# Kernel tuning notes

Hardware: AMD Instinct MI355X
Metric: run time of the kernel (lower is better)

Reference implementation:

```python
import jax, jax.numpy as jnp
import numpy as np

WINDOW_SIZE = 11
C1 = (0.01 * 255) ** 2
C2 = (0.03 * 255) ** 2


def _make_window():
    # NOTE: faithful to the torch module: Gaussian with 2*sigma^2 = 4, UNNORMALIZED.
    x = np.arange(WINDOW_SIZE)
    g = np.exp(-((x - WINDOW_SIZE // 2) ** 2) / float(2 * 2)).astype(np.float32)
    w2d = np.outer(g, g)  # [11, 11]
    return jnp.asarray(w2d)[None, None, :, :]  # OIHW = [1, 1, 11, 11]


def _conv(x, w):
    pad = WINDOW_SIZE // 2
    return jax.lax.conv_general_dilated(
        x, w, window_strides=(1, 1), padding=[(pad, pad), (pad, pad)],
        dimension_numbers=('NCHW', 'OIHW', 'NCHW'))


def setup_inputs() -> dict:
    key = jax.random.key(0)
    k1, k2 = jax.random.split(key)
    shape = (32, 1, 512, 512)
    img1 = jax.random.uniform(k1, shape, dtype=jnp.float32)
    img2 = jax.random.uniform(k2, shape, dtype=jnp.float32)
    return {"img1": img1, "img2": img2}


def reference(img1, img2):
    w = _make_window()
    mu1 = _conv(img1, w)
    mu2 = _conv(img2, w)
    mu1_sq = mu1 * mu1
    mu2_sq = mu2 * mu2
    mu1_mu2 = mu1 * mu2
    sigma1_sq = _conv(img1 * img1, w) - mu1_sq
    sigma2_sq = _conv(img2 * img2, w) - mu2_sq
    sigma12 = _conv(img1 * img2, w) - mu1_mu2
    ssim_map = ((2 * mu1_mu2 + C1) * (2 * sigma12 + C2)) / (
        (mu1_sq + mu2_sq + C1) * (sigma1_sq + sigma2_sq + C2))
    return jnp.mean((1.0 - ssim_map) / 2.0)
```

## Files before the change

kernel.cpp:

```cpp
#include <hip/hip_runtime.h>
#include <hip/hip_fp16.h>


#define IMGW 512
#define IMGH 512
#define NIMG 32
#define TW 32
#define TH 64
#define IN_H 74
#define IN_W 44
#define NPIX (IN_H * IN_W)
#define NCHUNK (IN_H * 11)
#define NBX 16
#define NBY 8
#define NBLOCKS (NBX * NBY * NIMG)
#define LOWCH 512
#define LOWROWS 42

typedef __attribute__((address_space(1))) const uint32_t ga_u32;
typedef __attribute__((address_space(3))) uint32_t ls_u32;

__device__ __forceinline__ void load16_lds(const float* g, float* l) {
  __builtin_amdgcn_global_load_lds((ga_u32*)g, (ls_u32*)l, 16, 0, 0);
}
__device__ __forceinline__ __half2 h2_of(uint32_t w) {
  return __builtin_bit_cast(__half2, w);
}
__device__ __forceinline__ uint32_t u_of(__half2 h) {
  return __builtin_bit_cast(uint32_t, h);
}
__device__ __forceinline__ void lds_barrier() {
  asm volatile("s_waitcnt lgkmcnt(0)" ::: "memory");
  __builtin_amdgcn_s_barrier();
  __builtin_amdgcn_sched_barrier(0);
}

__global__ __launch_bounds__(256, 4) void ssim_main(
    const float* __restrict__ img1, const float* __restrict__ img2,
    float* __restrict__ partial) {
  __shared__ uint32_t uRaw[NPIX * 2];
  __shared__ uint32_t sPK[NPIX];
  __shared__ float sWave[4];
  float* sA = (float*)uRaw;
  float* sB = (float*)(uRaw + NPIX);
  uint32_t* hAB = uRaw;
  uint32_t* hPM = uRaw + NPIX;

  constexpr float g[11] = {0.0019304541f, 0.018315639f, 0.10539922f,
                           0.36787944f,   0.7788008f,   1.0f,
                           0.7788008f,    0.36787944f,  0.10539922f,
                           0.018315639f,  0.0019304541f};
  constexpr float C1v = 6.5025f;
  constexpr float C2v = 58.5225f;

  __half2 gh[11];
#pragma unroll
  for (int k = 0; k < 11; ++k) gh[k] = __float2half2_rn(g[k]);
  const __half2 c1m1 = __floats2half2_rn(1.0f, -1.0f);

  const int tid = threadIdx.x;
  const int bid = blockIdx.x;
  const int wgid = (bid & 7) * (NBLOCKS / 8) + (bid >> 3);
  const int img = wgid >> 7;
  const int by = (wgid >> 4) & 7;
  const int bx = wgid & 15;
  const int x0 = bx * TW - 5;
  const int y0 = by * TH - 5;
  const float* __restrict__ p1 = img1 + (size_t)img * (IMGW * IMGH);
  const float* __restrict__ p2 = img2 + (size_t)img * (IMGW * IMGH);
  const bool borderBlk =
      (bx == 0) || (bx == NBX - 1) || (by == 0) || (by == NBY - 1);

#pragma unroll
  for (int i = 0; i < 4; ++i) {
    int ch = tid + 256 * i;
    if (ch < NCHUNK) {
      int r = ch / 11;
      int cg = ch - r * 11;
      int gy = y0 + r;
      int gx = x0 + 4 * cg;
      int gyc = min(max(gy, 0), IMGH - 1);
      int gxc = min(max(gx, 0), IMGW - 4);
      int src = gyc * IMGW + gxc;
      load16_lds(p1 + src, &sA[ch * 4]);
      load16_lds(p2 + src, &sB[ch * 4]);
    }
  }
  asm volatile("s_waitcnt vmcnt(2)" ::: "memory");
  __builtin_amdgcn_s_barrier();
  __builtin_amdgcn_sched_barrier(0);

  auto prepass = [&](int cbeg, int cend) {
    if (!borderBlk) {
      for (int ch = cbeg + tid; ch < cend; ch += 256) {
        float4 a = *(const float4*)&sA[ch * 4];
        float4 b = *(const float4*)&sB[ch * 4];
        uint4 w;
        w.x = u_of(__floats2half2_rn(a.x, b.x));
        w.y = u_of(__floats2half2_rn(a.y, b.y));
        w.z = u_of(__floats2half2_rn(a.z, b.z));
        w.w = u_of(__floats2half2_rn(a.w, b.w));
        *(uint4*)&sPK[ch * 4] = w;
      }
    } else {
      for (int ch = cbeg + tid; ch < cend; ch += 256) {
        int r = ch / 11;
        int cg = ch - r * 11;
        int gy = y0 + r;
        int gx = x0 + 4 * cg;
        float4 a = *(const float4*)&sA[ch * 4];
        float4 b = *(const float4*)&sB[ch * 4];
        bool rowok = (gy >= 0) && (gy < IMGH);
        uint4 w;
        float av[4] = {a.x, a.y, a.z, a.w};
        float bv[4] = {b.x, b.y, b.z, b.w};
        uint32_t* wp = (uint32_t*)&w;
#pragma unroll
        for (int j = 0; j < 4; ++j) {
          bool ok = rowok && (gx + j >= 0) && (gx + j < IMGW);
          wp[j] = u_of(__floats2half2_rn(ok ? av[j] : 0.f, ok ? bv[j] : 0.f));
        }
        *(uint4*)&sPK[ch * 4] = w;
      }
    }
  };

  auto stage2 = [&](int rowbase, int nrows) {
    for (int idx = tid; idx < nrows * 8; idx += 256) {
      int r = rowbase + (idx >> 3);
      int c0 = (idx & 7) << 2;
      int base = r * IN_W + c0;
      __half2 ab[14], pm2[14];
      {
        uint4 w0 = *(const uint4*)&sPK[base];
        uint4 w1 = *(const uint4*)&sPK[base + 4];
        uint4 w2 = *(const uint4*)&sPK[base + 8];
        uint2 w3 = *(const uint2*)&sPK[base + 12];
        uint32_t ws[14] = {w0.x, w0.y, w0.z, w0.w, w1.x, w1.y, w1.z,
                           w1.w, w2.x, w2.y, w2.z, w2.w, w3.x, w3.y};
#pragma unroll
        for (int k = 0; k < 14; ++k) {
          __half2 w = h2_of(ws[k]);
          ab[k] = w;
          __half2 t = __hfma2(__lowhigh2highlow(w), c1m1, w);
          pm2[k] = __hmul2(t, t);
        }
      }
      uint4 oab, opm;
#pragma unroll
      for (int o = 0; o < 4; ++o) {
        __half2 cab = __float2half2_rn(0.0f);
        __half2 cpm = __float2half2_rn(0.0f);
#pragma unroll
        for (int k = 0; k < 11; ++k) {
          cab = __hfma2(gh[k], ab[o + k], cab);
          cpm = __hfma2(gh[k], pm2[o + k], cpm);
        }
        ((uint32_t*)&oab)[o] = u_of(cab);
        ((uint32_t*)&opm)[o] = u_of(cpm);
      }
      *(uint4*)&hAB[r * 32 + c0] = oab;
      *(uint4*)&hPM[r * 32 + c0] = opm;
    }
  };

  prepass(0, LOWCH);
  lds_barrier();
  stage2(0, LOWROWS);
  asm volatile("s_waitcnt vmcnt(0) lgkmcnt(0)" ::: "memory");
  __builtin_amdgcn_s_barrier();
  __builtin_amdgcn_sched_barrier(0);
  prepass(LOWCH, NCHUNK);
  lds_barrier();
  stage2(LOWROWS, IN_H - LOWROWS);
  lds_barrier();

  const int c = tid & 31;
  const int r0 = (tid >> 5) << 3;
  __half2 mAB[8], mPM[8];
  {
    __half2 m1[18], m2[18];
#pragma unroll
    for (int k = 0; k < 18; ++k) {
      m1[k] = h2_of(hAB[(r0 + k) * 32 + c]);
      m2[k] = h2_of(hPM[(r0 + k) * 32 + c]);
    }
#pragma unroll
    for (int o = 0; o < 8; ++o) {
      __half2 s = __float2half2_rn(0.0f);
      __half2 t = __float2half2_rn(0.0f);
#pragma unroll
      for (int k = 0; k < 11; ++k) {
        s = __hfma2(gh[k], m1[o + k], s);
        t = __hfma2(gh[k], m2[o + k], t);
      }
      mAB[o] = s; mPM[o] = t;
    }
  }

  float ssum = 0.f;
#pragma unroll
  for (int o = 0; o < 8; ++o) {
    float m1 = __low2float(mAB[o]);
    float m2 = __high2float(mAB[o]);
    float qp = __low2float(mPM[o]);
    float qm = __high2float(mPM[o]);
    float sumsq = 0.5f * (qp + qm);
    float eab = 0.25f * (qp - qm);
    float m1s = m1 * m1, m2s = m2 * m2, m12 = m1 * m2;
    float sg12 = eab - m12;
    float sgsum = sumsq - m1s - m2s;
    float num = (2.0f * m12 + C1v) * (2.0f * sg12 + C2v);
    float den = (m1s + m2s + C1v) * (sgsum + C2v);
    float r = num * __builtin_amdgcn_rcpf(den);
    if (!__builtin_isfinite(r)) r = 0.0f;
    ssum += r;
  }

#pragma unroll
  for (int off = 32; off > 0; off >>= 1) ssum += __shfl_down(ssum, off, 64);
  if ((tid & 63) == 0) sWave[tid >> 6] = ssum;
  __syncthreads();
  if (tid == 0) {
    partial[wgid] = sWave[0] + sWave[1] + sWave[2] + sWave[3];
  }
}

__global__ __launch_bounds__(256) void ssim_reduce(
    const float* __restrict__ partial, float* __restrict__ out) {
  const int tid = threadIdx.x;
  float s = 0.f;
  for (int i = tid; i < NBLOCKS; i += 256) s += partial[i];
#pragma unroll
  for (int off = 32; off > 0; off >>= 1) s += __shfl_down(s, off, 64);
  __shared__ float sw[4];
  if ((tid & 63) == 0) sw[tid >> 6] = s;
  __syncthreads();
  if (tid == 0) {
    float tot = sw[0] + sw[1] + sw[2] + sw[3];
    float val = 0.5f * (1.0f - tot * (1.0f / (32.0f * 512.0f * 512.0f)));
    if (!__builtin_isfinite(val)) val = 0.0f;
    out[0] = val;
  }
}

extern "C" void kernel_launch(void* const* d_in, const int* in_sizes, int n_in,
                              void* d_out, int out_size, void* d_ws,
                              size_t ws_size, hipStream_t stream) {
  const float* img1 = (const float*)d_in[0];
  const float* img2 = (const float*)d_in[1];
  float* partial = (float*)d_ws;
  float* out = (float*)d_out;

  hipLaunchKernelGGL(ssim_main, dim3(NBLOCKS), dim3(256), 0, stream, img1,
                     img2, partial);
  hipLaunchKernelGGL(ssim_reduce, dim3(1), dim3(256), 0, stream, partial, out);
}
```

Before: 40.94 us.

## Widen horizontal pass, retile vertical pass, and compute SSIM epilogue in packed half

Each thread in the horizontal blur now produces 8 outputs instead of 4, which amortizes the shared-memory loads and pair squaring over more outputs. The intermediate buffer gets a padded row stride of 36 to reduce bank conflicts. The vertical pass is retiled so each thread handles 2 columns by 4 rows, with the weights prescaled by 1/8 to keep values in fp16 range. The SSIM formula itself now runs in packed fp16 with rescaled constants, using perm to regroup lanes, and only the final division is done in fp32. The fp16 rescaling risks precision loss and overflow, and the LOWROWS split point is changed.

```diff
diff --git a/kernel.cpp b/kernel.cpp
--- a/kernel.cpp
+++ b/kernel.cpp
@@ -9,13 +9,14 @@
 #define TH 64
 #define IN_H 74
 #define IN_W 44
+#define HSTR 36
 #define NPIX (IN_H * IN_W)
 #define NCHUNK (IN_H * 11)
 #define NBX 16
 #define NBY 8
 #define NBLOCKS (NBX * NBY * NIMG)
 #define LOWCH 512
-#define LOWROWS 42
+#define LOWROWS 46
 
 typedef __attribute__((address_space(1))) const uint32_t ga_u32;
 typedef __attribute__((address_space(3))) uint32_t ls_u32;
@@ -50,13 +51,19 @@
                            0.36787944f,   0.7788008f,   1.0f,
                            0.7788008f,    0.36787944f,  0.10539922f,
                            0.018315639f,  0.0019304541f};
-  constexpr float C1v = 6.5025f;
-  constexpr float C2v = 58.5225f;
-
-  __half2 gh[11];
-#pragma unroll
-  for (int k = 0; k < 11; ++k) gh[k] = __float2half2_rn(g[k]);
+
+  __half2 gh[11], gh8[11];
+#pragma unroll
+  for (int k = 0; k < 11; ++k) {
+    gh[k] = __float2half2_rn(g[k]);
+    gh8[k] = __float2half2_rn(g[k] * 0.125f);
+  }
   const __half2 c1m1 = __floats2half2_rn(1.0f, -1.0f);
+  const __half2 kQS = __float2half2_rn(0.0625f);
+  const __half2 kQD = __float2half2_rn(0.03125f);
+  const __half2 C1s = __float2half2_rn(6.5025f / 64.0f);
+  const __half2 C2s = __float2half2_rn(58.5225f / 64.0f);
+  const __half2 htwo = __float2half2_rn(2.0f);
 
   const int tid = threadIdx.x;
   const int bid = blockIdx.x;
@@ -126,29 +133,31 @@
   };
 
   auto stage2 = [&](int rowbase, int nrows) {
-    for (int idx = tid; idx < nrows * 8; idx += 256) {
-      int r = rowbase + (idx >> 3);
-      int c0 = (idx & 7) << 2;
+    for (int idx = tid; idx < nrows * 4; idx += 256) {
+      int r = rowbase + (idx >> 2);
+      int c0 = (idx & 3) << 3;
       int base = r * IN_W + c0;
-      __half2 ab[14], pm2[14];
+      __half2 ab[18], pm2[18];
       {
         uint4 w0 = *(const uint4*)&sPK[base];
         uint4 w1 = *(const uint4*)&sPK[base + 4];
         uint4 w2 = *(const uint4*)&sPK[base + 8];
-        uint2 w3 = *(const uint2*)&sPK[base + 12];
-        uint32_t ws[14] = {w0.x, w0.y, w0.z, w0.w, w1.x, w1.y, w1.z,
-                           w1.w, w2.x, w2.y, w2.z, w2.w, w3.x, w3.y};
-#pragma unroll
-        for (int k = 0; k < 14; ++k) {
+        uint4 w3 = *(const uint4*)&sPK[base + 12];
+        uint2 w4 = *(const uint2*)&sPK[base + 16];
+        uint32_t ws[18] = {w0.x, w0.y, w0.z, w0.w, w1.x, w1.y, w1.z, w1.w,
+                           w2.x, w2.y, w2.z, w2.w, w3.x, w3.y, w3.z, w3.w,
+                           w4.x, w4.y};
+#pragma unroll
+        for (int k = 0; k < 18; ++k) {
           __half2 w = h2_of(ws[k]);
           ab[k] = w;
           __half2 t = __hfma2(__lowhigh2highlow(w), c1m1, w);
           pm2[k] = __hmul2(t, t);
         }
       }
-      uint4 oab, opm;
-#pragma unroll
-      for (int o = 0; o < 4; ++o) {
+      uint32_t oab[8], opm[8];
+#pragma unroll
+      for (int o = 0; o < 8; ++o) {
         __half2 cab = __float2half2_rn(0.0f);
         __half2 cpm = __float2half2_rn(0.0f);
 #pragma unroll
@@ -156,11 +165,14 @@
           cab = __hfma2(gh[k], ab[o + k], cab);
           cpm = __hfma2(gh[k], pm2[o + k], cpm);
         }
-        ((uint32_t*)&oab)[o] = u_of(cab);
-        ((uint32_t*)&opm)[o] = u_of(cpm);
-      }
-      *(uint4*)&hAB[r * 32 + c0] = oab;
-      *(uint4*)&hPM[r * 32 + c0] = opm;
+        oab[o] = u_of(cab);
+        opm[o] = u_of(cpm);
+      }
+      int hb = r * HSTR + c0;
+      *(uint4*)&hAB[hb] = make_uint4(oab[0], oab[1], oab[2], oab[3]);
+      *(uint4*)&hAB[hb + 4] = make_uint4(oab[4], oab[5], oab[6], oab[7]);
+      *(uint4*)&hPM[hb] = make_uint4(opm[0], opm[1], opm[2], opm[3]);
+      *(uint4*)&hPM[hb + 4] = make_uint4(opm[4], opm[5], opm[6], opm[7]);
     }
   };
 
@@ -175,46 +187,62 @@
   stage2(LOWROWS, IN_H - LOWROWS);
   lds_barrier();
 
-  const int c = tid & 31;
-  const int r0 = (tid >> 5) << 3;
-  __half2 mAB[8], mPM[8];
-  {
-    __half2 m1[18], m2[18];
-#pragma unroll
-    for (int k = 0; k < 18; ++k) {
-      m1[k] = h2_of(hAB[(r0 + k) * 32 + c]);
-      m2[k] = h2_of(hPM[(r0 + k) * 32 + c]);
-    }
-#pragma unroll
-    for (int o = 0; o < 8; ++o) {
-      __half2 s = __float2half2_rn(0.0f);
-      __half2 t = __float2half2_rn(0.0f);
-#pragma unroll
-      for (int k = 0; k < 11; ++k) {
-        s = __hfma2(gh[k], m1[o + k], s);
-        t = __hfma2(gh[k], m2[o + k], t);
-      }
-      mAB[o] = s; mPM[o] = t;
+  const int cp = tid & 15;
+  const int rg = tid >> 4;
+  const int r0 = rg << 2;
+  __half2 aAB0[4], aAB1[4], aPM0[4], aPM1[4];
+#pragma unroll
+  for (int o = 0; o < 4; ++o) {
+    aAB0[o] = __float2half2_rn(0.f);
+    aAB1[o] = __float2half2_rn(0.f);
+    aPM0[o] = __float2half2_rn(0.f);
+    aPM1[o] = __float2half2_rn(0.f);
+  }
+#pragma unroll
+  for (int k = 0; k < 14; ++k) {
+    int row = r0 + k;
+    uint2 ab = *(const uint2*)&hAB[row * HSTR + 2 * cp];
+    uint2 pm = *(const uint2*)&hPM[row * HSTR + 2 * cp];
+#pragma unroll
+    for (int o = 0; o < 4; ++o) {
+      if (k - o >= 0 && k - o <= 10) {
+        aAB0[o] = __hfma2(gh8[k - o], h2_of(ab.x), aAB0[o]);
+        aAB1[o] = __hfma2(gh8[k - o], h2_of(ab.y), aAB1[o]);
+        aPM0[o] = __hfma2(gh8[k - o], h2_of(pm.x), aPM0[o]);
+        aPM1[o] = __hfma2(gh8[k - o], h2_of(pm.y), aPM1[o]);
+      }
     }
   }
 
   float ssum = 0.f;
 #pragma unroll
-  for (int o = 0; o < 8; ++o) {
-    float m1 = __low2float(mAB[o]);
-    float m2 = __high2float(mAB[o]);
-    float qp = __low2float(mPM[o]);
-    float qm = __high2float(mPM[o]);
-    float sumsq = 0.5f * (qp + qm);
-    float eab = 0.25f * (qp - qm);
-    float m1s = m1 * m1, m2s = m2 * m2, m12 = m1 * m2;
-    float sg12 = eab - m12;
-    float sgsum = sumsq - m1s - m2s;
-    float num = (2.0f * m12 + C1v) * (2.0f * sg12 + C2v);
-    float den = (m1s + m2s + C1v) * (sgsum + C2v);
-    float r = num * __builtin_amdgcn_rcpf(den);
-    if (!__builtin_isfinite(r)) r = 0.0f;
-    ssum += r;
+  for (int o = 0; o < 4; ++o) {
+    uint32_t uab0 = u_of(aAB0[o]), uab1 = u_of(aAB1[o]);
+    uint32_t upm0 = u_of(aPM0[o]), upm1 = u_of(aPM1[o]);
+    __half2 M1 = h2_of(__builtin_amdgcn_perm(uab1, uab0, 0x05040100));
+    __half2 M2 = h2_of(__builtin_amdgcn_perm(uab1, uab0, 0x07060302));
+    __half2 QP = h2_of(__builtin_amdgcn_perm(upm1, upm0, 0x05040100));
+    __half2 QM = h2_of(__builtin_amdgcn_perm(upm1, upm0, 0x07060302));
+    __half2 m12 = __hmul2(M1, M2);
+    __half2 s1q = __hmul2(M1, M1);
+    __half2 s2q = __hmul2(M2, M2);
+    __half2 sumsq = __hmul2(__hadd2(QP, QM), kQS);
+    __half2 eab = __hmul2(__hsub2(QP, QM), kQD);
+    __half2 sg12 = __hsub2(eab, m12);
+    __half2 sgsum = __hsub2(__hsub2(sumsq, s1q), s2q);
+    __half2 numA = __hfma2(m12, htwo, C1s);
+    __half2 numB = __hfma2(sg12, htwo, C2s);
+    __half2 num = __hmul2(numA, numB);
+    __half2 denA = __hadd2(__hadd2(s1q, s2q), C1s);
+    __half2 denB = __hadd2(sgsum, C2s);
+    __half2 den = __hmul2(denA, denB);
+    float nlo = __low2float(num), nhi = __high2float(num);
+    float dlo = __low2float(den), dhi = __high2float(den);
+    float ra = nlo * __builtin_amdgcn_rcpf(dlo);
+    float rb = nhi * __builtin_amdgcn_rcpf(dhi);
+    if (!__builtin_isfinite(ra)) ra = 0.f;
+    if (!__builtin_isfinite(rb)) rb = 0.f;
+    ssum += ra + rb;
   }
 
 #pragma unroll
```

New measurement: 39.78 us. 1.03x faster.
